# Kernel optimization log

Hardware: AMD Instinct MI355X
Metric: run time of the kernel (lower is better)

## Reference

```python
import jax, jax.numpy as jnp
import numpy as np

EMBED_DIM = 128
HEADS = 4
HEAD_DIM = EMBED_DIM // HEADS
HIDDEN = EMBED_DIM * 4


def setup_inputs() -> dict:
    key = jax.random.key(0)
    ks = jax.random.split(key, 12)
    s = 0.02
    return {
        "x": jax.random.normal(ks[0], (4, 4096, EMBED_DIM), dtype=jnp.float32),
        "ln1_g": jnp.ones((EMBED_DIM,), jnp.float32),
        "ln1_b": jnp.zeros((EMBED_DIM,), jnp.float32),
        "qkv_w": jax.random.normal(ks[1], (EMBED_DIM, 3 * EMBED_DIM), jnp.float32) * s,
        "qkv_b": jnp.zeros((3 * EMBED_DIM,), jnp.float32),
        "proj_w": jax.random.normal(ks[2], (EMBED_DIM, EMBED_DIM), jnp.float32) * s,
        "proj_b": jnp.zeros((EMBED_DIM,), jnp.float32),
        "ln2_g": jnp.ones((EMBED_DIM,), jnp.float32),
        "ln2_b": jnp.zeros((EMBED_DIM,), jnp.float32),
        "mlp_w1": jax.random.normal(ks[3], (EMBED_DIM, HIDDEN), jnp.float32) * s,
        "mlp_b1": jnp.zeros((HIDDEN,), jnp.float32),
        "mlp_w2": jax.random.normal(ks[4], (HIDDEN, EMBED_DIM), jnp.float32) * s,
        "mlp_b2": jnp.zeros((EMBED_DIM,), jnp.float32),
    }


def _layernorm(x, g, b, eps=1e-5):
    mu = jnp.mean(x, axis=-1, keepdims=True)
    var = jnp.var(x, axis=-1, keepdims=True)
    return (x - mu) * jax.lax.rsqrt(var + eps) * g + b


def _msa(x, qkv_w, qkv_b, proj_w, proj_b):
    B, N, C = x.shape
    qkv = x @ qkv_w + qkv_b                       # [B,N,3C]
    qkv = qkv.reshape(B, N, 3, HEADS, HEAD_DIM)
    q, k, v = jnp.moveaxis(qkv, 2, 0)             # each [B,N,H,D]
    # scores: [B,H,N,N]
    attn = jnp.einsum("bnhd,bmhd->bhnm", q, k) / jnp.sqrt(jnp.float32(HEAD_DIM))
    attn = jax.nn.softmax(attn, axis=-1)
    out = jnp.einsum("bhnm,bmhd->bnhd", attn, v).reshape(B, N, C)
    return out @ proj_w + proj_b


def reference(x, ln1_g, ln1_b, qkv_w, qkv_b, proj_w, proj_b,
              ln2_g, ln2_b, mlp_w1, mlp_b1, mlp_w2, mlp_b2):
    # dropout is identity in eval mode
    x = x + _msa(_layernorm(x, ln1_g, ln1_b), qkv_w, qkv_b, proj_w, proj_b)
    h = _layernorm(x, ln2_g, ln2_b)
    h = jax.nn.gelu(h @ mlp_w1 + mlp_b1, approximate=False)
    x = x + (h @ mlp_w2 + mlp_b2)
    return x
```

## Files before the change

### kernel.cpp

```cpp
#include <hip/hip_runtime.h>
#include <hip/hip_bf16.h>
#include <math.h>

#define NSEQ   4096
#define CDIM   128
#define HD     32

typedef __attribute__((ext_vector_type(8))) short short8;
typedef __attribute__((ext_vector_type(4))) short short4v;
typedef __attribute__((ext_vector_type(4))) float f32x4;

#define QSCL (0.17677669529663687f * 1.4426950408889634f)

__device__ inline unsigned short f2bf(float f){
  union { float f; unsigned u; } v; v.f = f;
  return (unsigned short)((v.u + 0x7fffu + ((v.u >> 16) & 1u)) >> 16);
}
__device__ inline float bf2f(unsigned short u){
  union { unsigned u; float f; } v; v.u = ((unsigned)u) << 16;
  return v.f;
}
__device__ inline void gload_lds16(const unsigned short* g, unsigned short* l){
  __builtin_amdgcn_global_load_lds(
      (const __attribute__((address_space(1))) void*)g,
      (__attribute__((address_space(3))) void*)l, 16, 0, 0);
}


__global__ __launch_bounds__(256) void k_pack(
    const float* __restrict__ qkv_w, const float* __restrict__ qkv_b,
    const float* __restrict__ proj_w, const float* __restrict__ mlp_w1,
    const float* __restrict__ mlp_w2, unsigned short* __restrict__ wpack,
    float* __restrict__ bqs)
{
  const int gt = blockIdx.x * 256 + threadIdx.x;
  const int tile = gt >> 6, lane = gt & 63;
  const float* src; int N, KT, toff, dstoff; float scale = 1.f;
  if (tile < 96)       { src = qkv_w;  N = 384; KT = 4;  toff = tile;       dstoff = 0; }
  else if (tile < 128) { src = proj_w; N = 128; KT = 4;  toff = tile - 96;  dstoff = 49152; }
  else if (tile < 256) { src = mlp_w1; N = 512; KT = 4;  toff = tile - 128; dstoff = 65536; }
  else                 { src = mlp_w2; N = 128; KT = 16; toff = tile - 256; dstoff = 131072; }
  const int ct = toff / KT, kt = toff % KT;
  if (tile < 96 && ct < 8) scale = QSCL;
  const int row0 = kt * 32 + (lane >> 4) * 8, col = ct * 16 + (lane & 15);
  short8 v;
  #pragma unroll
  for (int i = 0; i < 8; i++)
    v[i] = (short)f2bf(src[(size_t)(row0 + i) * N + col] * scale);
  *(short8*)(wpack + dstoff + ((size_t)(ct * KT + kt) * 64 + lane) * 8) = v;
  if (gt < 384) bqs[gt] = qkv_b[gt] * (gt < 128 ? QSCL : 1.f);
}

__global__ __launch_bounds__(512) void k_qkv(
    const float* __restrict__ x, const float* __restrict__ g,
    const float* __restrict__ b, const unsigned short* __restrict__ wpack,
    const float* __restrict__ bqs, unsigned short* __restrict__ qkv)
{
  __shared__ unsigned short xn[64 * 128];
  const int tid = threadIdx.x;
  const int tok0 = blockIdx.x * 64;
  {
    const int grp = tid >> 5, l = tid & 31;
    #pragma unroll
    for (int it = 0; it < 4; it++){
      const int t = it * 16 + grp;
      const float4 xv = *(const float4*)(x + (size_t)(tok0 + t) * 128 + l * 4);
      float s  = xv.x + xv.y + xv.z + xv.w;
      float s2 = xv.x*xv.x + xv.y*xv.y + xv.z*xv.z + xv.w*xv.w;
      #pragma unroll
      for (int m = 1; m <= 16; m <<= 1){ s += __shfl_xor(s, m); s2 += __shfl_xor(s2, m); }
      const float mu = s * (1.f/128.f);
      const float rs = rsqrtf(s2 * (1.f/128.f) - mu*mu + 1e-5f);
      const int e = l * 4;
      const float4 gv = *(const float4*)(g + e), bv = *(const float4*)(b + e);
      short4v pk;
      pk[0] = (short)f2bf((xv.x - mu)*rs*gv.x + bv.x);
      pk[1] = (short)f2bf((xv.y - mu)*rs*gv.y + bv.y);
      pk[2] = (short)f2bf((xv.z - mu)*rs*gv.z + bv.z);
      pk[3] = (short)f2bf((xv.w - mu)*rs*gv.w + bv.w);
      const int bl = l >> 1;
      const int slot = bl * 64 + (t & 48) + ((t & 15) ^ bl);
      *(short4v*)(xn + slot * 8 + (l & 1) * 4) = pk;
    }
  }
  __syncthreads();
  const int wv = tid >> 6, lane = tid & 63, r = lane & 15, cg = lane >> 4;
  const int rt = wv & 3, ct0 = (wv >> 2) * 12;
  short8 af[4];
  #pragma unroll
  for (int kt = 0; kt < 4; kt++){
    const int bl = kt * 4 + cg;
    const int slot = bl * 64 + rt * 16 + (r ^ bl);
    af[kt] = *(const short8*)(xn + slot * 8);
  }
  const int bidx = tok0 >> 12, nloc = (tok0 & (NSEQ - 1)) + rt * 16 + cg * 4;
  for (int ct = ct0; ct < ct0 + 12; ct++){
    f32x4 acc = {0.f, 0.f, 0.f, 0.f};
    const unsigned short* bp = wpack + ((size_t)(ct * 4) * 64 + lane) * 8;
    #pragma unroll
    for (int kt = 0; kt < 4; kt++)
      acc = __builtin_amdgcn_mfma_f32_16x16x32_bf16(af[kt], *(const short8*)(bp + kt * 512), acc, 0, 0, 0);
    const int col = ct * 16 + r;
    const float bi = bqs[col];
    if (ct < 8){
      const int cc = col & 127, h = cc >> 5, d = cc & 31;
      unsigned short* plane = qkv + ((size_t)bidx * 4 + h) * (NSEQ * HD);
      #pragma unroll
      for (int reg = 0; reg < 4; reg++)
        plane[(size_t)(nloc + reg) * HD + d] = f2bf(acc[reg] + bi);
    } else if (ct < 16){
      const int cc = col & 127, h = cc >> 5, d = cc & 31;
      unsigned short* plane = qkv + ((size_t)16 + bidx * 4 + h) * (NSEQ * HD);
      const int t16 = ((tok0 & (NSEQ - 1)) >> 4) + rt;
      #pragma unroll
      for (int reg = 0; reg < 4; reg++)
        plane[(size_t)t16 * 512 + (d >> 3) * 128 + (cg * 4 + reg) * 8 + (d & 7)]
            = f2bf(acc[reg] + bi);
    } else {
      const int vct = ct - 16, h = vct >> 1, half = vct & 1;
      unsigned short* plane = qkv + ((size_t)32 + bidx * 4 + h) * (NSEQ * HD);
      const size_t ntile = (size_t)((tok0 & (NSEQ - 1)) >> 5) + (rt >> 1);
      const size_t vo = (ntile * 2 + half) * 512 + lane * 8 + (rt & 1) * 4;
      short4v pk;
      #pragma unroll
      for (int reg = 0; reg < 4; reg++) pk[reg] = (short)f2bf(acc[reg] + bi);
      *(short4v*)(plane + vo) = pk;
    }
  }
}

__global__ __launch_bounds__(256, 8) void k_attn(
    const unsigned short* __restrict__ qkv, unsigned short* __restrict__ part_ob,
    float* __restrict__ part_l)
{
  __shared__ unsigned short sbuf[8192];
  const int tid = threadIdx.x;
  const int lane = tid & 63, wv = tid >> 6;
  const int chunk = blockIdx.y, bh = blockIdx.z;
  const int qbase = blockIdx.x * 128 + wv * 32;
  const int kv0 = chunk * 1024;
  const unsigned short* Q  = qkv + (size_t)bh * (NSEQ * HD);
  const unsigned short* Kc = qkv + (size_t)(16 + bh) * (NSEQ * HD) + (size_t)kv0 * HD;
  const unsigned short* Vc = qkv + (size_t)(32 + bh) * (NSEQ * HD) + (size_t)kv0 * HD;
  const int r = lane & 15, cg = lane >> 4;
  const short8 qf0 = *(const short8*)(Q + (size_t)(qbase + r) * HD + cg * 8);
  const short8 qf1 = *(const short8*)(Q + (size_t)(qbase + 16 + r) * HD + cg * 8);
  const unsigned short* gsrc = (wv < 2 ? Kc : Vc) + (size_t)(wv & 1) * 512 + lane * 8;
  const int dst_off = ((wv >> 1) & 1) * 1024 + (wv & 1) * 512;
  union { unsigned u[4]; short8 s; } onesu;
  onesu.u[0] = 0x3F803F80u; onesu.u[1] = 0x3F803F80u;
  onesu.u[2] = 0x3F803F80u; onesu.u[3] = 0x3F803F80u;
  const short8 vones = onesu.s;
  f32x4 o00 = {0.f,0.f,0.f,0.f}, o01 = {0.f,0.f,0.f,0.f};
  f32x4 o10 = {0.f,0.f,0.f,0.f}, o11 = {0.f,0.f,0.f,0.f};
  f32x4 lacc0 = {0.f,0.f,0.f,0.f}, lacc1 = {0.f,0.f,0.f,0.f};
  const f32x4 zero = {0.f,0.f,0.f,0.f};
  gload_lds16(gsrc,        sbuf + 0 * 2048 + dst_off);
  gload_lds16(gsrc + 1024, sbuf + 1 * 2048 + dst_off);
  gload_lds16(gsrc + 2048, sbuf + 2 * 2048 + dst_off);
  for (int t = 0; t < 32; t++){
    asm volatile("s_waitcnt vmcnt(2) lgkmcnt(0)" ::: "memory");
    __builtin_amdgcn_sched_barrier(0);
    __builtin_amdgcn_s_barrier();
    __builtin_amdgcn_sched_barrier(0);
    const int tn = (t + 3 > 31) ? 31 : t + 3;
    gload_lds16(gsrc + (size_t)tn * 1024, sbuf + ((t + 3) & 3) * 2048 + dst_off);
    const unsigned short* skb = sbuf + (t & 3) * 2048;
    const unsigned short* svb = skb + 1024;
    const short8 ka0 = *(const short8*)(skb + lane * 8);
    const short8 ka1 = *(const short8*)(skb + 512 + lane * 8);
    const short8 va0 = *(const short8*)(svb + lane * 8);
    const short8 va1 = *(const short8*)(svb + 512 + lane * 8);
    const f32x4 s00 = __builtin_amdgcn_mfma_f32_16x16x32_bf16(ka0, qf0, zero, 0, 0, 0);
    const f32x4 s01 = __builtin_amdgcn_mfma_f32_16x16x32_bf16(ka1, qf0, zero, 0, 0, 0);
    const f32x4 s10 = __builtin_amdgcn_mfma_f32_16x16x32_bf16(ka0, qf1, zero, 0, 0, 0);
    const f32x4 s11 = __builtin_amdgcn_mfma_f32_16x16x32_bf16(ka1, qf1, zero, 0, 0, 0);
    float p00[4], p01[4], p10[4], p11[4];
    #pragma unroll
    for (int i = 0; i < 4; i++){
      p00[i] = __builtin_amdgcn_exp2f(s00[i]);
      p01[i] = __builtin_amdgcn_exp2f(s01[i]);
      p10[i] = __builtin_amdgcn_exp2f(s10[i]);
      p11[i] = __builtin_amdgcn_exp2f(s11[i]);
    }
    unsigned c0, c1, c2, c3, c4, c5, c6, c7;
    asm("v_cvt_pk_bf16_f32 %0, %1, %2" : "=v"(c0) : "v"(p00[0]), "v"(p00[1]));
    asm("v_cvt_pk_bf16_f32 %0, %1, %2" : "=v"(c1) : "v"(p00[2]), "v"(p00[3]));
    asm("v_cvt_pk_bf16_f32 %0, %1, %2" : "=v"(c2) : "v"(p01[0]), "v"(p01[1]));
    asm("v_cvt_pk_bf16_f32 %0, %1, %2" : "=v"(c3) : "v"(p01[2]), "v"(p01[3]));
    asm("v_cvt_pk_bf16_f32 %0, %1, %2" : "=v"(c4) : "v"(p10[0]), "v"(p10[1]));
    asm("v_cvt_pk_bf16_f32 %0, %1, %2" : "=v"(c5) : "v"(p10[2]), "v"(p10[3]));
    asm("v_cvt_pk_bf16_f32 %0, %1, %2" : "=v"(c6) : "v"(p11[0]), "v"(p11[1]));
    asm("v_cvt_pk_bf16_f32 %0, %1, %2" : "=v"(c7) : "v"(p11[2]), "v"(p11[3]));
    union { unsigned u[4]; short8 s; } pa, pb;
    pa.u[0] = c0; pa.u[1] = c1; pa.u[2] = c2; pa.u[3] = c3;
    pb.u[0] = c4; pb.u[1] = c5; pb.u[2] = c6; pb.u[3] = c7;
    o00 = __builtin_amdgcn_mfma_f32_16x16x32_bf16(va0, pa.s, o00, 0, 0, 0);
    o01 = __builtin_amdgcn_mfma_f32_16x16x32_bf16(va1, pa.s, o01, 0, 0, 0);
    o10 = __builtin_amdgcn_mfma_f32_16x16x32_bf16(va0, pb.s, o10, 0, 0, 0);
    o11 = __builtin_amdgcn_mfma_f32_16x16x32_bf16(va1, pb.s, o11, 0, 0, 0);
    lacc0 = __builtin_amdgcn_mfma_f32_16x16x32_bf16(vones, pa.s, lacc0, 0, 0, 0);
    lacc1 = __builtin_amdgcn_mfma_f32_16x16x32_bf16(vones, pb.s, lacc1, 0, 0, 0);
  }
  asm volatile("s_waitcnt vmcnt(0)" ::: "memory");
  const float ls0 = lacc0[0], ls1 = lacc1[0];
  unsigned short* po = part_ob + (((size_t)(chunk * 16 + bh) * NSEQ) + qbase + r) * HD;
  short4v w0, w1, w2, w3;
  #pragma unroll
  for (int j = 0; j < 4; j++){
    w0[j] = (short)f2bf(o00[j]); w1[j] = (short)f2bf(o01[j]);
    w2[j] = (short)f2bf(o10[j]); w3[j] = (short)f2bf(o11[j]);
  }
  *(short4v*)(po + cg * 4)              = w0;
  *(short4v*)(po + 16 + cg * 4)         = w1;
  *(short4v*)(po + 16 * HD + cg * 4)    = w2;
  *(short4v*)(po + 16 * HD + 16 + cg * 4) = w3;
  if (lane < 16){
    part_l[(size_t)(chunk * 16 + bh) * NSEQ + qbase + r] = ls0;
    part_l[(size_t)(chunk * 16 + bh) * NSEQ + qbase + 16 + r] = ls1;
  }
}

__global__ __launch_bounds__(512, 2) void k_fused(
    const unsigned short* __restrict__ part_ob, const float* __restrict__ part_l,
    const float* __restrict__ x, const unsigned short* __restrict__ wpack,
    const float* __restrict__ pb, const float* __restrict__ g2,
    const float* __restrict__ b2, const float* __restrict__ b1,
    const float* __restrict__ b2m, float* __restrict__ out)
{
  __shared__ float sb[32 * 128];
  __shared__ unsigned short hfr[2][2048];
  __shared__ unsigned short afr[2][8192];
  const int tid = threadIdx.x, tok0 = blockIdx.x * 32;
  const int wv = tid >> 6, lane = tid & 63, r = lane & 15, cg = lane >> 4;
  const int rt = wv & 1, cgp = wv >> 1;
  const int bidx = tok0 >> 12, qn0 = (tok0 & (NSEQ - 1)) + rt * 16 + r;
  short8 af[4];
  #pragma unroll
  for (int kt = 0; kt < 4; kt++){
    const int bh = bidx * 4 + kt;
    float s8[8] = {0.f,0.f,0.f,0.f,0.f,0.f,0.f,0.f};
    float lsum = 0.f;
    #pragma unroll
    for (int c = 0; c < 4; c++){
      const short8 v = *(const short8*)(part_ob +
          (((size_t)(c * 16 + bh) * NSEQ) + qn0) * HD + cg * 8);
      #pragma unroll
      for (int i = 0; i < 8; i++) s8[i] += bf2f((unsigned short)v[i]);
      lsum += part_l[(size_t)(c * 16 + bh) * NSEQ + qn0];
    }
    const float inv = 1.f / lsum;
    #pragma unroll
    for (int i = 0; i < 8; i++) af[kt][i] = (short)f2bf(s8[i] * inv);
  }
  {
    const unsigned short* wp = wpack + 49152;
    for (int ct = cgp * 2; ct < cgp * 2 + 2; ct++){
      f32x4 acc = {0.f, 0.f, 0.f, 0.f};
      const unsigned short* bp = wp + ((size_t)(ct * 4) * 64 + lane) * 8;
      #pragma unroll
      for (int kt = 0; kt < 4; kt++)
        acc = __builtin_amdgcn_mfma_f32_16x16x32_bf16(af[kt], *(const short8*)(bp + kt * 512), acc, 0, 0, 0);
      const int col = ct * 16 + r;
      const float bi = pb[col];
      #pragma unroll
      for (int reg = 0; reg < 4; reg++){
        const int tl = rt * 16 + cg * 4 + reg;
        sb[tl * 128 + col] = acc[reg] + bi + x[(size_t)(tok0 + tl) * 128 + col];
      }
    }
  }
  __syncthreads();
  {
    const int grp = tid >> 5, l = tid & 31;
    #pragma unroll
    for (int it = 0; it < 2; it++){
      const int t = it * 16 + grp;
      const float4 xv = *(const float4*)(sb + t * 128 + l * 4);
      float s  = xv.x + xv.y + xv.z + xv.w;
      float s2 = xv.x*xv.x + xv.y*xv.y + xv.z*xv.z + xv.w*xv.w;
      #pragma unroll
      for (int m = 1; m <= 16; m <<= 1){ s += __shfl_xor(s, m); s2 += __shfl_xor(s2, m); }
      const float mu = s * (1.f/128.f);
      const float rs = rsqrtf(s2 * (1.f/128.f) - mu*mu + 1e-5f);
      const int e = l * 4;
      const float4 gv = *(const float4*)(g2 + e), bv = *(const float4*)(b2 + e);
      short4v pk;
      pk[0] = (short)f2bf((xv.x - mu)*rs*gv.x + bv.x);
      pk[1] = (short)f2bf((xv.y - mu)*rs*gv.y + bv.y);
      pk[2] = (short)f2bf((xv.z - mu)*rs*gv.z + bv.z);
      pk[3] = (short)f2bf((xv.w - mu)*rs*gv.w + bv.w);
      *(short4v*)(&hfr[t >> 4][(e >> 3) * 128 + (t & 15) * 8 + (e & 7)]) = pk;
    }
  }
  __syncthreads();
  {
    short8 hf[4];
    #pragma unroll
    for (int kt = 0; kt < 4; kt++)
      hf[kt] = *(const short8*)(&hfr[rt][(kt * 4 + cg) * 128 + r * 8]);
    const unsigned short* w1 = wpack + 65536;
    for (int ct = cgp * 8; ct < cgp * 8 + 8; ct++){
      f32x4 acc = {0.f, 0.f, 0.f, 0.f};
      const unsigned short* bp = w1 + ((size_t)(ct * 4) * 64 + lane) * 8;
      #pragma unroll
      for (int kt = 0; kt < 4; kt++)
        acc = __builtin_amdgcn_mfma_f32_16x16x32_bf16(hf[kt], *(const short8*)(bp + kt * 512), acc, 0, 0, 0);
      const int col = ct * 16 + r;
      const float bi = b1[col];
      #pragma unroll
      for (int reg = 0; reg < 4; reg++){
        const float v = acc[reg] + bi;
        const float ge = 0.5f * v * (1.f + erff(v * 0.70710678118f));
        afr[rt][(col >> 3) * 128 + (cg * 4 + reg) * 8 + (col & 7)] = f2bf(ge);
      }
    }
  }
  __syncthreads();
  {
    const unsigned short* w2 = wpack + 131072;
    f32x4 acc0 = {0.f,0.f,0.f,0.f}, acc1 = {0.f,0.f,0.f,0.f};
    for (int kt = 0; kt < 16; kt++){
      const short8 a3 = *(const short8*)(&afr[rt][(kt * 4 + cg) * 128 + r * 8]);
      const unsigned short* bp0 = w2 + ((size_t)((cgp * 2 + 0) * 16 + kt) * 64 + lane) * 8;
      const unsigned short* bp1 = w2 + ((size_t)((cgp * 2 + 1) * 16 + kt) * 64 + lane) * 8;
      acc0 = __builtin_amdgcn_mfma_f32_16x16x32_bf16(a3, *(const short8*)(bp0), acc0, 0, 0, 0);
      acc1 = __builtin_amdgcn_mfma_f32_16x16x32_bf16(a3, *(const short8*)(bp1), acc1, 0, 0, 0);
    }
    #pragma unroll
    for (int c = 0; c < 2; c++){
      const f32x4 acc = c ? acc1 : acc0;
      const int col = (cgp * 2 + c) * 16 + r;
      const float bi = b2m[col];
      #pragma unroll
      for (int reg = 0; reg < 4; reg++){
        const int tl = rt * 16 + cg * 4 + reg;
        out[(size_t)(tok0 + tl) * 128 + col] = acc[reg] + bi + sb[tl * 128 + col];
      }
    }
  }
}

extern "C" void kernel_launch(void* const* d_in, const int* in_sizes, int n_in,
                              void* d_out, int out_size, void* d_ws, size_t ws_size,
                              hipStream_t stream)
{
  const float* x      = (const float*)d_in[0];
  const float* ln1_g  = (const float*)d_in[1];
  const float* ln1_b  = (const float*)d_in[2];
  const float* qkv_w  = (const float*)d_in[3];
  const float* qkv_b  = (const float*)d_in[4];
  const float* proj_w = (const float*)d_in[5];
  const float* proj_b = (const float*)d_in[6];
  const float* ln2_g  = (const float*)d_in[7];
  const float* ln2_b  = (const float*)d_in[8];
  const float* mlp_w1 = (const float*)d_in[9];
  const float* mlp_b1 = (const float*)d_in[10];
  const float* mlp_w2 = (const float*)d_in[11];
  const float* mlp_b2 = (const float*)d_in[12];

  char* ws = (char*)d_ws;
  unsigned short* wpack   = (unsigned short*)(ws);
  float*          bqs     = (float*)(ws + 393216);
  unsigned short* qkv     = (unsigned short*)(ws + 524288);
  unsigned short* part_ob = (unsigned short*)(ws + 13107200);
  float*          part_l  = (float*)(ws + 29884416);
  float* out = (float*)d_out;

  hipLaunchKernelGGL(k_pack, dim3(96), dim3(256), 0, stream,
                     qkv_w, qkv_b, proj_w, mlp_w1, mlp_w2, wpack, bqs);
  hipLaunchKernelGGL(k_qkv, dim3(256), dim3(512), 0, stream,
                     x, ln1_g, ln1_b, wpack, bqs, qkv);
  hipLaunchKernelGGL(k_attn, dim3(32, 4, 16), dim3(256), 0, stream,
                     qkv, part_ob, part_l);
  hipLaunchKernelGGL(k_fused, dim3(512), dim3(512), 0, stream,
                     part_ob, part_l, x, wpack, proj_b, ln2_g, ln2_b,
                     mlp_b1, mlp_b2, out);
}
```

Baseline: 89.53 us.

## Halve KV split count and double KV tile per attention step

```diff
diff --git a/kernel.cpp b/kernel.cpp
--- a/kernel.cpp
+++ b/kernel.cpp
@@ -129,24 +129,25 @@
   }
 }
 
-__global__ __launch_bounds__(256, 8) void k_attn(
+__global__ __launch_bounds__(256, 4) void k_attn(
     const unsigned short* __restrict__ qkv, unsigned short* __restrict__ part_ob,
     float* __restrict__ part_l)
 {
-  __shared__ unsigned short sbuf[8192];
+  __shared__ unsigned short sbuf[16384];
   const int tid = threadIdx.x;
   const int lane = tid & 63, wv = tid >> 6;
   const int chunk = blockIdx.y, bh = blockIdx.z;
   const int qbase = blockIdx.x * 128 + wv * 32;
-  const int kv0 = chunk * 1024;
+  const int kv0 = chunk * 2048;
   const unsigned short* Q  = qkv + (size_t)bh * (NSEQ * HD);
   const unsigned short* Kc = qkv + (size_t)(16 + bh) * (NSEQ * HD) + (size_t)kv0 * HD;
   const unsigned short* Vc = qkv + (size_t)(32 + bh) * (NSEQ * HD) + (size_t)kv0 * HD;
   const int r = lane & 15, cg = lane >> 4;
   const short8 qf0 = *(const short8*)(Q + (size_t)(qbase + r) * HD + cg * 8);
   const short8 qf1 = *(const short8*)(Q + (size_t)(qbase + 16 + r) * HD + cg * 8);
-  const unsigned short* gsrc = (wv < 2 ? Kc : Vc) + (size_t)(wv & 1) * 512 + lane * 8;
-  const int dst_off = ((wv >> 1) & 1) * 1024 + (wv & 1) * 512;
+  const unsigned short* gK = Kc + wv * 512 + lane * 8;
+  const unsigned short* gV = Vc + wv * 512 + lane * 8;
+  const int dK = wv * 512, dV = 2048 + wv * 512;
   union { unsigned u[4]; short8 s; } onesu;
   onesu.u[0] = 0x3F803F80u; onesu.u[1] = 0x3F803F80u;
   onesu.u[2] = 0x3F803F80u; onesu.u[3] = 0x3F803F80u;
@@ -155,52 +156,59 @@
   f32x4 o10 = {0.f,0.f,0.f,0.f}, o11 = {0.f,0.f,0.f,0.f};
   f32x4 lacc0 = {0.f,0.f,0.f,0.f}, lacc1 = {0.f,0.f,0.f,0.f};
   const f32x4 zero = {0.f,0.f,0.f,0.f};
-  gload_lds16(gsrc,        sbuf + 0 * 2048 + dst_off);
-  gload_lds16(gsrc + 1024, sbuf + 1 * 2048 + dst_off);
-  gload_lds16(gsrc + 2048, sbuf + 2 * 2048 + dst_off);
+  gload_lds16(gK,        sbuf + 0 * 4096 + dK);
+  gload_lds16(gV,        sbuf + 0 * 4096 + dV);
+  gload_lds16(gK + 2048, sbuf + 1 * 4096 + dK);
+  gload_lds16(gV + 2048, sbuf + 1 * 4096 + dV);
+  gload_lds16(gK + 4096, sbuf + 2 * 4096 + dK);
+  gload_lds16(gV + 4096, sbuf + 2 * 4096 + dV);
   for (int t = 0; t < 32; t++){
-    asm volatile("s_waitcnt vmcnt(2) lgkmcnt(0)" ::: "memory");
+    asm volatile("s_waitcnt vmcnt(4) lgkmcnt(0)" ::: "memory");
     __builtin_amdgcn_sched_barrier(0);
     __builtin_amdgcn_s_barrier();
     __builtin_amdgcn_sched_barrier(0);
     const int tn = (t + 3 > 31) ? 31 : t + 3;
-    gload_lds16(gsrc + (size_t)tn * 1024, sbuf + ((t + 3) & 3) * 2048 + dst_off);
-    const unsigned short* skb = sbuf + (t & 3) * 2048;
-    const unsigned short* svb = skb + 1024;
-    const short8 ka0 = *(const short8*)(skb + lane * 8);
-    const short8 ka1 = *(const short8*)(skb + 512 + lane * 8);
-    const short8 va0 = *(const short8*)(svb + lane * 8);
-    const short8 va1 = *(const short8*)(svb + 512 + lane * 8);
-    const f32x4 s00 = __builtin_amdgcn_mfma_f32_16x16x32_bf16(ka0, qf0, zero, 0, 0, 0);
-    const f32x4 s01 = __builtin_amdgcn_mfma_f32_16x16x32_bf16(ka1, qf0, zero, 0, 0, 0);
-    const f32x4 s10 = __builtin_amdgcn_mfma_f32_16x16x32_bf16(ka0, qf1, zero, 0, 0, 0);
-    const f32x4 s11 = __builtin_amdgcn_mfma_f32_16x16x32_bf16(ka1, qf1, zero, 0, 0, 0);
-    float p00[4], p01[4], p10[4], p11[4];
-    #pragma unroll
-    for (int i = 0; i < 4; i++){
-      p00[i] = __builtin_amdgcn_exp2f(s00[i]);
-      p01[i] = __builtin_amdgcn_exp2f(s01[i]);
-      p10[i] = __builtin_amdgcn_exp2f(s10[i]);
-      p11[i] = __builtin_amdgcn_exp2f(s11[i]);
-    }
-    unsigned c0, c1, c2, c3, c4, c5, c6, c7;
-    asm("v_cvt_pk_bf16_f32 %0, %1, %2" : "=v"(c0) : "v"(p00[0]), "v"(p00[1]));
-    asm("v_cvt_pk_bf16_f32 %0, %1, %2" : "=v"(c1) : "v"(p00[2]), "v"(p00[3]));
-    asm("v_cvt_pk_bf16_f32 %0, %1, %2" : "=v"(c2) : "v"(p01[0]), "v"(p01[1]));
-    asm("v_cvt_pk_bf16_f32 %0, %1, %2" : "=v"(c3) : "v"(p01[2]), "v"(p01[3]));
-    asm("v_cvt_pk_bf16_f32 %0, %1, %2" : "=v"(c4) : "v"(p10[0]), "v"(p10[1]));
-    asm("v_cvt_pk_bf16_f32 %0, %1, %2" : "=v"(c5) : "v"(p10[2]), "v"(p10[3]));
-    asm("v_cvt_pk_bf16_f32 %0, %1, %2" : "=v"(c6) : "v"(p11[0]), "v"(p11[1]));
-    asm("v_cvt_pk_bf16_f32 %0, %1, %2" : "=v"(c7) : "v"(p11[2]), "v"(p11[3]));
-    union { unsigned u[4]; short8 s; } pa, pb;
-    pa.u[0] = c0; pa.u[1] = c1; pa.u[2] = c2; pa.u[3] = c3;
-    pb.u[0] = c4; pb.u[1] = c5; pb.u[2] = c6; pb.u[3] = c7;
-    o00 = __builtin_amdgcn_mfma_f32_16x16x32_bf16(va0, pa.s, o00, 0, 0, 0);
-    o01 = __builtin_amdgcn_mfma_f32_16x16x32_bf16(va1, pa.s, o01, 0, 0, 0);
-    o10 = __builtin_amdgcn_mfma_f32_16x16x32_bf16(va0, pb.s, o10, 0, 0, 0);
-    o11 = __builtin_amdgcn_mfma_f32_16x16x32_bf16(va1, pb.s, o11, 0, 0, 0);
-    lacc0 = __builtin_amdgcn_mfma_f32_16x16x32_bf16(vones, pa.s, lacc0, 0, 0, 0);
-    lacc1 = __builtin_amdgcn_mfma_f32_16x16x32_bf16(vones, pb.s, lacc1, 0, 0, 0);
+    gload_lds16(gK + (size_t)tn * 2048, sbuf + ((t + 3) & 3) * 4096 + dK);
+    gload_lds16(gV + (size_t)tn * 2048, sbuf + ((t + 3) & 3) * 4096 + dV);
+    const unsigned short* skb = sbuf + (t & 3) * 4096;
+    const unsigned short* svb = skb + 2048;
+    #pragma unroll
+    for (int ktp = 0; ktp < 2; ktp++){
+      const short8 kaa = *(const short8*)(skb + (ktp * 2 + 0) * 512 + lane * 8);
+      const short8 kab = *(const short8*)(skb + (ktp * 2 + 1) * 512 + lane * 8);
+      const short8 va0 = *(const short8*)(svb + (ktp * 2 + 0) * 512 + lane * 8);
+      const short8 va1 = *(const short8*)(svb + (ktp * 2 + 1) * 512 + lane * 8);
+      const f32x4 s00 = __builtin_amdgcn_mfma_f32_16x16x32_bf16(kaa, qf0, zero, 0, 0, 0);
+      const f32x4 s01 = __builtin_amdgcn_mfma_f32_16x16x32_bf16(kab, qf0, zero, 0, 0, 0);
+      const f32x4 s10 = __builtin_amdgcn_mfma_f32_16x16x32_bf16(kaa, qf1, zero, 0, 0, 0);
+      const f32x4 s11 = __builtin_amdgcn_mfma_f32_16x16x32_bf16(kab, qf1, zero, 0, 0, 0);
+      float p00[4], p01[4], p10[4], p11[4];
+      #pragma unroll
+      for (int i = 0; i < 4; i++){
+        p00[i] = __builtin_amdgcn_exp2f(s00[i]);
+        p01[i] = __builtin_amdgcn_exp2f(s01[i]);
+        p10[i] = __builtin_amdgcn_exp2f(s10[i]);
+        p11[i] = __builtin_amdgcn_exp2f(s11[i]);
+      }
+      unsigned c0, c1, c2, c3, c4, c5, c6, c7;
+      asm("v_cvt_pk_bf16_f32 %0, %1, %2" : "=v"(c0) : "v"(p00[0]), "v"(p00[1]));
+      asm("v_cvt_pk_bf16_f32 %0, %1, %2" : "=v"(c1) : "v"(p00[2]), "v"(p00[3]));
+      asm("v_cvt_pk_bf16_f32 %0, %1, %2" : "=v"(c2) : "v"(p01[0]), "v"(p01[1]));
+      asm("v_cvt_pk_bf16_f32 %0, %1, %2" : "=v"(c3) : "v"(p01[2]), "v"(p01[3]));
+      asm("v_cvt_pk_bf16_f32 %0, %1, %2" : "=v"(c4) : "v"(p10[0]), "v"(p10[1]));
+      asm("v_cvt_pk_bf16_f32 %0, %1, %2" : "=v"(c5) : "v"(p10[2]), "v"(p10[3]));
+      asm("v_cvt_pk_bf16_f32 %0, %1, %2" : "=v"(c6) : "v"(p11[0]), "v"(p11[1]));
+      asm("v_cvt_pk_bf16_f32 %0, %1, %2" : "=v"(c7) : "v"(p11[2]), "v"(p11[3]));
+      union { unsigned u[4]; short8 s; } pa, pb;
+      pa.u[0] = c0; pa.u[1] = c1; pa.u[2] = c2; pa.u[3] = c3;
+      pb.u[0] = c4; pb.u[1] = c5; pb.u[2] = c6; pb.u[3] = c7;
+      o00 = __builtin_amdgcn_mfma_f32_16x16x32_bf16(va0, pa.s, o00, 0, 0, 0);
+      o01 = __builtin_amdgcn_mfma_f32_16x16x32_bf16(va1, pa.s, o01, 0, 0, 0);
+      o10 = __builtin_amdgcn_mfma_f32_16x16x32_bf16(va0, pb.s, o10, 0, 0, 0);
+      o11 = __builtin_amdgcn_mfma_f32_16x16x32_bf16(va1, pb.s, o11, 0, 0, 0);
+      lacc0 = __builtin_amdgcn_mfma_f32_16x16x32_bf16(vones, pa.s, lacc0, 0, 0, 0);
+      lacc1 = __builtin_amdgcn_mfma_f32_16x16x32_bf16(vones, pb.s, lacc1, 0, 0, 0);
+    }
   }
   asm volatile("s_waitcnt vmcnt(0)" ::: "memory");
   const float ls0 = lacc0[0], ls1 = lacc1[0];
@@ -242,7 +250,7 @@
     float s8[8] = {0.f,0.f,0.f,0.f,0.f,0.f,0.f,0.f};
     float lsum = 0.f;
     #pragma unroll
-    for (int c = 0; c < 4; c++){
+    for (int c = 0; c < 2; c++){
       const short8 v = *(const short8*)(part_ob +
           (((size_t)(c * 16 + bh) * NSEQ) + qn0) * HD + cg * 8);
       #pragma unroll
@@ -371,7 +379,7 @@
                      qkv_w, qkv_b, proj_w, mlp_w1, mlp_w2, wpack, bqs);
   hipLaunchKernelGGL(k_qkv, dim3(256), dim3(512), 0, stream,
                      x, ln1_g, ln1_b, wpack, bqs, qkv);
-  hipLaunchKernelGGL(k_attn, dim3(32, 4, 16), dim3(256), 0, stream,
+  hipLaunchKernelGGL(k_attn, dim3(32, 2, 16), dim3(256), 0, stream,
                      qkv, part_ob, part_l);
   hipLaunchKernelGGL(k_fused, dim3(512), dim3(512), 0, stream,
                      part_ob, part_l, x, wpack, proj_b, ln2_g, ln2_b,
```

Result: faster. 82.78 us (-7.5%).
